# Optimization experiments

Measured on AMD Instinct MI355X. Metric: run time of the kernel, lower is better.

Reference implementation:

```python
import jax, jax.numpy as jnp
import numpy as np

B, S, D = 1, 1024, 1024
NH, DH, DR = 8, 128, 64
DCQ, DC = 768, 256
INTER, E, TOPK = 512, 8, 2

def rmsnorm(x, w, eps=1e-6):
    return x * jax.lax.rsqrt(jnp.mean(x * x, -1, keepdims=True) + eps) * w

def lin(x, w, b):
    return x @ w.T + b

def apply_rope(x, cos, sin):
    # x: [b, s, h, d]; cos/sin: [S, d//2]; complex rotate pairs (even, odd)
    b, s, h, d = x.shape
    xr = x.reshape(b, s, h, d // 2, 2)
    x0, x1 = xr[..., 0], xr[..., 1]
    c = cos[None, :s, None, :]
    sn = sin[None, :s, None, :]
    return jnp.stack([x0 * c - x1 * sn, x0 * sn + x1 * c], -1).reshape(b, s, h, d)

def setup_inputs():
    keys = iter(jax.random.split(jax.random.key(0), 64))
    def nrm(*shape):
        return jax.random.normal(next(keys), shape, jnp.float32) * 0.02
    theta = 1.0 / (10000.0 ** (jnp.arange(0, DR, 2, dtype=jnp.float32) / DR))
    ang = jnp.arange(S, dtype=jnp.float32)[:, None] * theta[None, :]
    return dict(
        h=jax.random.normal(next(keys), (B, S, D), jnp.float32),
        freqs_cos=jnp.cos(ang), freqs_sin=jnp.sin(ang),
        mask=jnp.triu(jnp.ones((S, S), bool), 1),
        attn_norm_w=jnp.ones(D), ffn_norm_w=jnp.ones(D),
        wq_down=nrm(DCQ, D), bq_down=jnp.zeros(DCQ), q_norm_w=jnp.ones(DCQ),
        wqc=nrm(NH * DH, DCQ), bqc=jnp.zeros(NH * DH),
        wqr=nrm(NH * DR, DCQ), bqr=jnp.zeros(NH * DR),
        wkr=nrm(DR, D), bkr=jnp.zeros(DR), kr_norm_w=jnp.ones(DR),
        wkv_down=nrm(DC, D), bkv_down=jnp.zeros(DC), kv_norm_w=jnp.ones(DC),
        wkc=nrm(NH * DH, DC), bkc=jnp.zeros(NH * DH),
        wvc=nrm(NH * DH, DC), bvc=jnp.zeros(NH * DH),
        wo=nrm(D, NH * DH), bo=jnp.zeros(D),
        sw1=nrm(INTER, D), sb1=jnp.zeros(INTER), sw2=nrm(D, INTER), sb2=jnp.zeros(D),
        sw3=nrm(INTER, D), sb3=jnp.zeros(INTER),
        ew1=nrm(E, INTER, D), eb1=jnp.zeros((E, INTER)), ew2=nrm(E, D, INTER), eb2=jnp.zeros((E, D)),
        ew3=nrm(E, INTER, D), eb3=jnp.zeros((E, INTER)),
        centroids=jax.random.normal(next(keys), (E, D), jnp.float32), biases=jnp.zeros(E),
    )

def _forward(h, freqs_cos, freqs_sin, mask, attn_norm_w, ffn_norm_w, wq_down, bq_down, q_norm_w, wqc, bqc, wqr, bqr, wkr, bkr, kr_norm_w, wkv_down, bkv_down, kv_norm_w, wkc, bkc, wvc, bvc, wo, bo, sw1, sb1, sw2, sb2, sw3, sb3, ew1, eb1, ew2, eb2, ew3, eb3, centroids, biases):
    b, s, _ = h.shape
    # --- pre-norm MLA attention ---
    x = rmsnorm(h, attn_norm_w)
    cQ = rmsnorm(lin(x, wq_down, bq_down), q_norm_w)
    qR = apply_rope(lin(cQ, wqr, bqr).reshape(b, s, NH, DR), freqs_cos, freqs_sin)
    qC = lin(cQ, wqc, bqc).reshape(b, s, NH, DH)
    q = jnp.concatenate([qC, qR], -1)                      # [b,s,NH,DH+DR]
    kR = apply_rope(rmsnorm(lin(x, wkr, bkr), kr_norm_w).reshape(b, s, 1, DR), freqs_cos, freqs_sin)
    cKV = rmsnorm(lin(x, wkv_down, bkv_down), kv_norm_w)
    kC = lin(cKV, wkc, bkc).reshape(b, s, NH, DH)
    vC = lin(cKV, wvc, bvc).reshape(b, s, NH, DH)
    k = jnp.concatenate([jnp.broadcast_to(kR, (b, s, NH, DR)), kC], -1)  # source order: [kR, kC]
    scores = jnp.einsum('bqhd,bkhd->bhqk', q, k) / jnp.sqrt(jnp.float32(DH + DR))
    scores = jnp.where(mask[None, None], jnp.finfo(scores.dtype).min, scores)
    attw = jax.nn.softmax(scores, -1)                      # dropout in eval mode = identity
    attn = jnp.einsum('bhqk,bkhd->bqhd', attw, vC).reshape(b, s, NH * DH)
    x1 = h + lin(attn, wo, bo)
    # --- pre-norm MoE FFN ---
    y = rmsnorm(x1, ffn_norm_w)
    shared = lin(jax.nn.silu(lin(y, sw1, sb1)) * lin(y, sw3, sb3), sw2, sb2)  # mean over 1 shared expert
    affinity = jax.nn.sigmoid(y @ centroids.T)             # [b,s,E]
    _, topi = jax.lax.top_k(affinity + biases, TOPK)
    gates = jax.nn.softmax(jnp.take_along_axis(affinity, topi, -1), -1)      # [b,s,TOPK]
    combine = (jax.nn.one_hot(topi, E, dtype=y.dtype) * gates[..., None]).sum(-2)  # [b,s,E]
    h1 = jax.nn.silu(jnp.einsum('bsd,eid->bsei', y, ew1) + eb1) * (jnp.einsum('bsd,eid->bsei', y, ew3) + eb3)
    out_e = jnp.einsum('bsei,edi->bsed', h1, ew2) + eb2
    routed = (out_e * combine[..., None]).sum(2)
    return x1 + shared + routed

def reference(h, freqs_cos, freqs_sin, mask, attn_norm_w, ffn_norm_w, wq_down, bq_down, q_norm_w, wqc, bqc, wqr, bqr, wkr, bkr, kr_norm_w, wkv_down, bkv_down, kv_norm_w, wkc, bkc, wvc, bvc, wo, bo, sw1, sb1, sw2, sb2, sw3, sb3, ew1, eb1, ew2, eb2, ew3, eb3, centroids, biases):
    return _forward(h, freqs_cos, freqs_sin, mask, attn_norm_w, ffn_norm_w, wq_down, bq_down, q_norm_w, wqc, bqc, wqr, bqr, wkr, bkr, kr_norm_w, wkv_down, bkv_down, kv_norm_w, wkc, bkc, wvc, bvc, wo, bo, sw1, sb1, sw2, sb2, sw3, sb3, ew1, eb1, ew2, eb2, ew3, eb3, centroids, biases)
```

## Files before the change

### kernel.cpp

```cpp
#include <hip/hip_runtime.h>

typedef unsigned short u16;
typedef __attribute__((ext_vector_type(8))) short short8;
typedef __attribute__((ext_vector_type(4))) float f32x4;

__device__ __forceinline__ float b2f(u16 u) { return __uint_as_float(((unsigned)u) << 16); }
__device__ __forceinline__ u16 f2b(float f) {
    unsigned x = __float_as_uint(f);
    return (u16)((x + 0x7fffu + ((x >> 16) & 1u)) >> 16);
}

#define GLDS16(gp, lp) __builtin_amdgcn_global_load_lds( \
    (const __attribute__((address_space(1))) void*)(gp), \
    (__attribute__((address_space(3))) void*)(lp), 16, 0, 0)

#define WAITV(N) do { \
    asm volatile("s_waitcnt vmcnt(" #N ")" ::: "memory"); \
    __builtin_amdgcn_sched_barrier(0); \
} while (0)

#define KC8_SWZ(lane) ((((lane) & 3) ^ (((lane) >> 3) & 3)) << 3)
#define RD_SWZ(fm, fq) (((fq) ^ (((fm) >> 1) & 3)) << 3)

__device__ __forceinline__ void xcd_swz(int& bx, int& by) {
    if ((gridDim.x & 7) == 0 && gridDim.y == 16) {
        int lid = bx + by * gridDim.x;
        int q = lid >> 3, r = lid & 7;
        by = q & 15;
        bx = r + ((q >> 4) << 3);
    }
}

struct Seg { const u16* W; const float* bias; void* C; int ldc; int epi; int bx0; int aidx; };
struct GArgs {
    const u16* A[2]; int lda[2]; int K[2];
    Seg seg[4]; int nseg;
    const float* res;
    float* dst2;
};

__launch_bounds__(256)
__global__ void mgemm4(GArgs ga)
{
    __shared__ u16 As[6 * 2048];
    __shared__ u16 Bs[6 * 2048];
    int bx = blockIdx.x, by = blockIdx.y;
    xcd_swz(bx, by);
    int si = 0;
#pragma unroll
    for (int i = 1; i < 4; i++)
        if (i < ga.nseg && bx >= ga.seg[i].bx0) si = i;
    const u16* Wp = ga.seg[si].W;
    const float* bp = ga.seg[si].bias;
    void* Cp = ga.seg[si].C;
    const int ldco = ga.seg[si].ldc;
    const int epi = ga.seg[si].epi;
    const int ai = ga.seg[si].aidx;
    const u16* Ap = ga.A[ai];
    const int lda = ga.lda[ai], K = ga.K[ai];
    const int col0 = (bx - ga.seg[si].bx0) * 64;
    const int row0 = by * 64;

    int tid = threadIdx.x;
    int lane = tid & 63, w = tid >> 6;
    int r0 = (w << 4) + (lane >> 2), kc8 = KC8_SWZ(lane);
    const u16* gA = Ap + (size_t)(row0 + r0) * lda + kc8;
    const u16* gB = Wp + (size_t)(col0 + r0) * lda + kc8;

    int fm = lane & 15, fq = lane >> 4;
    const int so = RD_SWZ(fm, fq);
    f32x4 acc[4] = {};

#define MG_STAGE(BS, KO) do { \
    GLDS16(gA + (KO), As + (BS) * 2048 + (w << 9)); \
    GLDS16(gB + (KO), Bs + (BS) * 2048 + (w << 9)); \
} while (0)

    const int nst = K >> 5;
    MG_STAGE(0, 0); MG_STAGE(1, 32); MG_STAGE(2, 64); MG_STAGE(3, 96);
    int bcur = 0;
    for (int t = 0; t < nst; t += 2) {
        if (t < nst - 2) { WAITV(4); } else { WAITV(0); }
        __builtin_amdgcn_s_barrier();
        int w4 = bcur + 4; if (w4 >= 6) w4 -= 6;
        int w5 = w4 + 1;   if (w5 >= 6) w5 -= 6;
        if (t + 4 < nst) MG_STAGE(w4, (t + 4) << 5);
        if (t + 5 < nst) MG_STAGE(w5, (t + 5) << 5);
#pragma unroll
        for (int sub = 0; sub < 2; sub++) {
            int bc = bcur + sub; if (bc >= 6) bc -= 6;
            short8 af = *(const short8*)(As + bc * 2048 + (w << 9) + fm * 32 + so);
            short8 bf[4];
#pragma unroll
            for (int nt = 0; nt < 4; nt++)
                bf[nt] = *(const short8*)(Bs + bc * 2048 + ((nt << 4) + fm) * 32 + so);
#pragma unroll
            for (int nt = 0; nt < 4; nt++)
                acc[nt] = __builtin_amdgcn_mfma_f32_16x16x32_bf16(af, bf[nt], acc[nt], 0, 0, 0);
        }
        bcur += 2; if (bcur >= 6) bcur -= 6;
    }
#undef MG_STAGE

    int rbase = row0 + (w << 4) + (fq << 2);
#pragma unroll
    for (int nt = 0; nt < 4; nt++) {
        int c = col0 + (nt << 4) + fm;
        float bcol = bp[c];
#pragma unroll
        for (int reg = 0; reg < 4; reg++) {
            int r = rbase + reg;
            float v = acc[nt][reg] + bcol;
            if (epi == 3)
                ((u16*)Cp)[(size_t)r * ldco + c] = f2b(v);
            else if (epi == 1) {
                float o = v + ga.res[(size_t)r * ldco + c];
                ((float*)Cp)[(size_t)r * ldco + c] = o;
                if (ga.dst2) ga.dst2[(size_t)r * ldco + c] = o;
            } else
                ((float*)Cp)[(size_t)r * ldco + c] = v;
        }
    }
}

__launch_bounds__(256)
__global__ void mega_glu(const u16* __restrict__ Y16,
                         const u16* __restrict__ sw1, const float* __restrict__ sb1,
                         const u16* __restrict__ sw3, const float* __restrict__ sb3,
                         const u16* __restrict__ ew1, const float* __restrict__ eb1,
                         const u16* __restrict__ ew3, const float* __restrict__ eb3,
                         u16* __restrict__ Gb,
                         const int* __restrict__ lists, const int* __restrict__ counts)
{
    __shared__ u16 As[6 * 2048];
    __shared__ u16 B1s[6 * 2048];
    __shared__ u16 B3s[6 * 2048];
    int bx = blockIdx.x, by = blockIdx.y, z = blockIdx.z;
    xcd_swz(bx, by);
    int col0 = bx * 64;
    int cnt = 1024; const int* list = nullptr;
    const u16 *W1p, *W3p; const float *b1p, *b3p;
    if (z == 0) {
        W1p = sw1; b1p = sb1; W3p = sw3; b3p = sb3;
    } else {
        int e = z - 1; cnt = counts[e]; list = lists + (e << 10);
        W1p = ew1 + (size_t)e * 512 * 1024; b1p = eb1 + e * 512;
        W3p = ew3 + (size_t)e * 512 * 1024; b3p = eb3 + e * 512;
    }
    int row0 = by * 64;
    if (row0 >= cnt) return;
    u16* Cp = Gb + (size_t)z * 524288;

    int tid = threadIdx.x, lane = tid & 63, w = tid >> 6;
    int r0 = (w << 4) + (lane >> 2), kc8 = KC8_SWZ(lane);
    int ar = row0 + r0;
    if (z > 0) ar = list[ar < cnt ? ar : cnt - 1];
    const u16* gA = Y16 + (size_t)ar * 1024 + kc8;
    const u16* gB1 = W1p + (size_t)(col0 + r0) * 1024 + kc8;
    const u16* gB3 = W3p + (size_t)(col0 + r0) * 1024 + kc8;

    int fm = lane & 15, fq = lane >> 4;
    const int so = RD_SWZ(fm, fq);
    f32x4 accU[4] = {}, accV[4] = {};

#define GL_STAGE(BS, KO) do { \
    GLDS16(gA + (KO),  As  + (BS) * 2048 + (w << 9)); \
    GLDS16(gB1 + (KO), B1s + (BS) * 2048 + (w << 9)); \
    GLDS16(gB3 + (KO), B3s + (BS) * 2048 + (w << 9)); \
} while (0)

    GL_STAGE(0, 0); GL_STAGE(1, 32); GL_STAGE(2, 64); GL_STAGE(3, 96);
    int bcur = 0;
    for (int t = 0; t < 32; t += 2) {
        if (t < 30) { WAITV(6); } else { WAITV(0); }
        __builtin_amdgcn_s_barrier();
        int w4 = bcur + 4; if (w4 >= 6) w4 -= 6;
        int w5 = w4 + 1;   if (w5 >= 6) w5 -= 6;
        if (t + 4 < 32) GL_STAGE(w4, (t + 4) << 5);
        if (t + 5 < 32) GL_STAGE(w5, (t + 5) << 5);
#pragma unroll
        for (int sub = 0; sub < 2; sub++) {
            int bc = bcur + sub; if (bc >= 6) bc -= 6;
            short8 af = *(const short8*)(As + bc * 2048 + (w << 9) + fm * 32 + so);
#pragma unroll
            for (int nt = 0; nt < 4; nt++) {
                short8 b1 = *(const short8*)(B1s + bc * 2048 + ((nt << 4) + fm) * 32 + so);
                accU[nt] = __builtin_amdgcn_mfma_f32_16x16x32_bf16(af, b1, accU[nt], 0, 0, 0);
            }
#pragma unroll
            for (int nt = 0; nt < 4; nt++) {
                short8 b3 = *(const short8*)(B3s + bc * 2048 + ((nt << 4) + fm) * 32 + so);
                accV[nt] = __builtin_amdgcn_mfma_f32_16x16x32_bf16(af, b3, accV[nt], 0, 0, 0);
            }
        }
        bcur += 2; if (bcur >= 6) bcur -= 6;
    }
#undef GL_STAGE

    int rbase = row0 + (w << 4) + (fq << 2);
#pragma unroll
    for (int nt = 0; nt < 4; nt++) {
        int c = col0 + (nt << 4) + fm;
        float b1c = b1p[c], b3c = b3p[c];
#pragma unroll
        for (int reg = 0; reg < 4; reg++) {
            int r = rbase + reg;
            if (r >= cnt) continue;
            float u = b2f(f2b(accU[nt][reg] + b1c));
            float v = b2f(f2b(accV[nt][reg] + b3c));
            Cp[(size_t)r * 512 + c] = f2b(u / (1.f + __expf(-u)) * v);
        }
    }
}

__launch_bounds__(256)
__global__ void mega_down(const u16* __restrict__ Gb,
                          const u16* __restrict__ sw2, const float* __restrict__ sb2,
                          const u16* __restrict__ ew2, const float* __restrict__ eb2,
                          float* __restrict__ Dscr,
                          const int* __restrict__ counts)
{
    __shared__ u16 Gs[6 * 2048];
    __shared__ u16 Ws[6 * 2048];
    int bx = blockIdx.x, by = blockIdx.y, z = blockIdx.z;
    xcd_swz(bx, by);
    int cnt = 1024;
    const u16* Wp; const float* bp;
    if (z == 0) { Wp = sw2; bp = sb2; }
    else {
        int e = z - 1;
        cnt = counts[e];
        Wp = ew2 + (size_t)e * 1024 * 512; bp = eb2 + e * 1024;
    }
    int row0 = by * 64;
    if (row0 >= cnt) return;
    const u16* Ap = Gb + (size_t)z * 524288;
    int col0 = bx * 64;
    float* Dp = Dscr + (size_t)z * 1048576;

    int tid = threadIdx.x, lane = tid & 63, w = tid >> 6;
    int r0 = (w << 4) + (lane >> 2), kc8 = KC8_SWZ(lane);
    const u16* gG = Ap + (size_t)(row0 + r0) * 512 + kc8;
    const u16* gW = Wp + (size_t)(col0 + r0) * 512 + kc8;

    int fm = lane & 15, fq = lane >> 4;
    const int so = RD_SWZ(fm, fq);
    f32x4 acc[4] = {};

#define MD_STAGE(BS, KO) do { \
    GLDS16(gG + (KO), Gs + (BS) * 2048 + (w << 9)); \
    GLDS16(gW + (KO), Ws + (BS) * 2048 + (w << 9)); \
} while (0)

    MD_STAGE(0, 0); MD_STAGE(1, 32); MD_STAGE(2, 64); MD_STAGE(3, 96);
    int bcur = 0;
    for (int t = 0; t < 16; t += 2) {
        if (t < 14) { WAITV(4); } else { WAITV(0); }
        __builtin_amdgcn_s_barrier();
        int w4 = bcur + 4; if (w4 >= 6) w4 -= 6;
        int w5 = w4 + 1;   if (w5 >= 6) w5 -= 6;
        if (t + 4 < 16) MD_STAGE(w4, (t + 4) << 5);
        if (t + 5 < 16) MD_STAGE(w5, (t + 5) << 5);
#pragma unroll
        for (int sub = 0; sub < 2; sub++) {
            int bc = bcur + sub; if (bc >= 6) bc -= 6;
            short8 af = *(const short8*)(Gs + bc * 2048 + (w << 9) + fm * 32 + so);
            short8 bf[4];
#pragma unroll
            for (int nt = 0; nt < 4; nt++)
                bf[nt] = *(const short8*)(Ws + bc * 2048 + ((nt << 4) + fm) * 32 + so);
#pragma unroll
            for (int nt = 0; nt < 4; nt++)
                acc[nt] = __builtin_amdgcn_mfma_f32_16x16x32_bf16(af, bf[nt], acc[nt], 0, 0, 0);
        }
        bcur += 2; if (bcur >= 6) bcur -= 6;
    }
#undef MD_STAGE

    int rbase = row0 + (w << 4) + (fq << 2);
#pragma unroll
    for (int nt = 0; nt < 4; nt++) {
        int c = col0 + (nt << 4) + fm;
        float bcol = bp[c];
#pragma unroll
        for (int reg = 0; reg < 4; reg++) {
            int r = rbase + reg;
            Dp[(size_t)r * 1024 + c] = acc[nt][reg] + bcol;
        }
    }
}

__launch_bounds__(256)
__global__ void ffn_combine(const float* __restrict__ Dscr,
                            const int* __restrict__ sE, const int* __restrict__ sP,
                            const float* __restrict__ sG,
                            float* __restrict__ out)
{
    int t = blockIdx.x, tid = threadIdx.x;
    int e0 = sE[t * 2], e1 = sE[t * 2 + 1];
    int p0 = sP[t * 2], p1 = sP[t * 2 + 1];
    float g0 = sG[t * 2], g1 = sG[t * 2 + 1];
    const float4* Ds = (const float4*)(Dscr + (size_t)t * 1024);
    const float4* D0 = (const float4*)(Dscr + (size_t)(e0 + 1) * 1048576 + (size_t)p0 * 1024);
    const float4* D1 = (const float4*)(Dscr + (size_t)(e1 + 1) * 1048576 + (size_t)p1 * 1024);
    float4* o = (float4*)(out + (size_t)t * 1024);
    float4 a = o[tid], s = Ds[tid], x0 = D0[tid], x1 = D1[tid];
    a.x += s.x + g0 * x0.x + g1 * x1.x;
    a.y += s.y + g0 * x0.y + g1 * x1.y;
    a.z += s.z + g0 * x0.z + g1 * x1.z;
    a.w += s.w + g0 * x0.w + g1 * x1.w;
    o[tid] = a;
}

__launch_bounds__(256)
__global__ void attn_mfma(const u16* __restrict__ Qp, const u16* __restrict__ Kp,
                          const u16* __restrict__ VT,
                          float* __restrict__ Opart, float* __restrict__ MLp)
{
    const int qt = blockIdx.x, h = blockIdx.y, z = blockIdx.z;
    const int q0 = qt * 64;
    const int tid = threadIdx.x;
    const int lane = tid & 63, w = tid >> 6;
    const int fm = lane & 15, fq = lane >> 4;

    __shared__ u16 Ks[12288];
    __shared__ u16 Vs[8192];
    __shared__ u16 Ps[4096];

    const u16* qrow = Qp + ((size_t)h * 1024 + q0 + w * 16 + fm) * 192;
    short8 qf[6];
#pragma unroll
    for (int c = 0; c < 6; c++)
        qf[c] = *(const short8*)(qrow + c * 32 + fq * 8);

    const u16* Kb = Kp + (size_t)h * 1024 * 192;
    const u16* Vb = VT + (size_t)h * 128 * 1024;

    float m_i[4], l_i[4];
#pragma unroll
    for (int r = 0; r < 4; r++) { m_i[r] = -1e30f; l_i[r] = 0.f; }
    f32x4 accO[8] = {};
    const float scale = 0.07216878364870323f;
    const int nt64 = qt + 1;
    const int ktlo = (z * nt64) >> 2;
    const int kthi = ((z + 1) * nt64) >> 2;
    const int rbase = w * 16 + fq * 4;

    for (int kt = ktlo; kt < kthi; ++kt) {
        const int o = kt * 64;
#pragma unroll
        for (int i = 0; i < 6; i++) {
            int idx = w + 4 * i;
            int c = idx >> 2, k4 = idx & 3;
            const u16* g = Kb + (size_t)(o + k4 * 16 + (lane >> 2)) * 192 + c * 32 + (lane & 3) * 8;
            GLDS16(g, Ks + c * 2048 + k4 * 512 + lane * 8);
        }
#pragma unroll
        for (int i = 0; i < 4; i++) {
            int idx = w + 4 * i;
            int kc = idx >> 3, k8 = idx & 7;
            const u16* g = Vb + (size_t)(k8 * 16 + (lane >> 2)) * 1024 + o + kc * 32 + (lane & 3) * 8;
            GLDS16(g, Vs + kc * 4096 + k8 * 512 + lane * 8);
        }
        __syncthreads();
        f32x4 sacc[4];
        __builtin_amdgcn_s_setprio(1);
#pragma unroll
        for (int nt = 0; nt < 4; nt++) {
            sacc[nt] = (f32x4){0.f, 0.f, 0.f, 0.f};
#pragma unroll
            for (int c = 0; c < 6; c++) {
                short8 kf = *(const short8*)(Ks + c * 2048 + (nt * 16 + fm) * 32 + fq * 8);
                sacc[nt] = __builtin_amdgcn_mfma_f32_16x16x32_bf16(qf[c], kf, sacc[nt], 0, 0, 0);
            }
        }
        __builtin_amdgcn_s_setprio(0);
        float pv[4][4], rmax[4];
#pragma unroll
        for (int reg = 0; reg < 4; reg++) {
            int q = q0 + rbase + reg;
            float mx = -1e30f;
#pragma unroll
            for (int nt = 0; nt < 4; nt++) {
                int gk = o + nt * 16 + fm;
                float s = sacc[nt][reg] * scale;
                if (gk > q) s = -1e30f;
                pv[nt][reg] = s;
                mx = fmaxf(mx, s);
            }
            rmax[reg] = mx;
        }
#pragma unroll
        for (int m = 1; m < 16; m <<= 1)
#pragma unroll
            for (int reg = 0; reg < 4; reg++)
                rmax[reg] = fmaxf(rmax[reg], __shfl_xor(rmax[reg], m));
        float alpha[4], rsum[4];
#pragma unroll
        for (int reg = 0; reg < 4; reg++) {
            float mn = fmaxf(m_i[reg], rmax[reg]);
            alpha[reg] = __expf(m_i[reg] - mn);
            m_i[reg] = mn;
// ... 149 lines not shown
            if (tid == 0) aff[e] = 1.f / (1.f + expf(-red[0] * scale));
            __syncthreads();
        }
        if (tid == 0) {
            float sb[8];
#pragma unroll
            for (int e = 0; e < 8; e++) sb[e] = aff[e] + biases[e];
            int i0 = 0;
            for (int e = 1; e < 8; e++) if (sb[e] > sb[i0]) i0 = e;
            int i1 = -1;
            for (int e = 0; e < 8; e++) { if (e == i0) continue; if (i1 < 0 || sb[e] > sb[i1]) i1 = e; }
            float a0 = aff[i0], a1 = aff[i1];
            float mx = fmaxf(a0, a1);
            float e0 = expf(a0 - mx), e1 = expf(a1 - mx);
            float inv = 1.f / (e0 + e1);
            int p0 = atomicAdd(&counts[i0], 1);
            lists[i0 * 1024 + p0] = t;
            int p1 = atomicAdd(&counts[i1], 1);
            lists[i1 * 1024 + p1] = t;
            sE[t * 2] = i0; sP[t * 2] = p0; sG[t * 2] = e0 * inv;
            sE[t * 2 + 1] = i1; sP[t * 2 + 1] = p1; sG[t * 2 + 1] = e1 * inv;
        }
    }
}

__launch_bounds__(256)
__global__ void pack_all(const float* __restrict__ QC, const float* __restrict__ QRr,
                         const float* __restrict__ KRraw, const float* __restrict__ krw,
                         const float* __restrict__ KC,
                         const u16* __restrict__ VCb,
                         const float* __restrict__ fcos, const float* __restrict__ fsin,
                         u16* __restrict__ Qp, u16* __restrict__ Kp, u16* __restrict__ VT)
{
    __shared__ u16 Ts[64][68];
    __shared__ float kshared[64];
    int b = blockIdx.x, tid = threadIdx.x;
    if (b < 1024) {
        int s = b;
        if (tid < 64) {
            float v = KRraw[(size_t)s * 64 + tid];
            float ss = v * v;
#pragma unroll
            for (int m = 1; m < 64; m <<= 1) ss += __shfl_xor(ss, m);
            float scale = rsqrtf(ss / 64.f + 1e-6f);
            int j = tid >> 1;
            float c = fcos[s * 32 + j], sn = fsin[s * 32 + j];
            float x0 = KRraw[(size_t)s * 64 + (tid & ~1)] * scale * krw[tid & ~1];
            float x1 = KRraw[(size_t)s * 64 + (tid | 1)]  * scale * krw[tid | 1];
            kshared[tid] = (tid & 1) ? (x0 * sn + x1 * c) : (x0 * c - x1 * sn);
        }
        __syncthreads();
        for (int e = tid; e < 1536; e += 256) {
            int h = e / 192, d = e % 192;
            float q;
            if (d < 128) {
                q = QC[(size_t)s * 1024 + h * 128 + d];
            } else {
                int dd = d - 128, j = dd >> 1;
                float c = fcos[s * 32 + j], sn = fsin[s * 32 + j];
                float x0 = QRr[(size_t)s * 512 + h * 64 + (dd & ~1)];
                float x1 = QRr[(size_t)s * 512 + h * 64 + (dd | 1)];
                q = (dd & 1) ? (x0 * sn + x1 * c) : (x0 * c - x1 * sn);
            }
            Qp[((size_t)h * 1024 + s) * 192 + d] = f2b(q);
            float k = (d < 64) ? kshared[d]
                               : KC[(size_t)s * 1024 + h * 128 + d - 64];
            Kp[((size_t)h * 1024 + s) * 192 + d] = f2b(k);
        }
    } else {
        int idx = b - 1024;
        int s0 = (idx & 15) * 64, d0 = (idx >> 4) * 64;
        for (int k = 0; k < 16; k++) {
            int e = tid + k * 256, r = e >> 6, c = e & 63;
            Ts[r][c] = VCb[(size_t)(s0 + r) * 1024 + d0 + c];
        }
        __syncthreads();
        for (int k = 0; k < 16; k++) {
            int e = tid + k * 256, d = e >> 6, s = e & 63;
            VT[(size_t)(d0 + d) * 1024 + s0 + s] = Ts[s][d];
        }
    }
}

#define NCAST 4096
__launch_bounds__(256)
__global__ void fused_cast(const float* p0, const float* p1, const float* p2,
                           const float* p3, const float* p4, const float* p5,
                           const float* p6, const float* p7, const float* p8,
                           const float* p9, const float* p10, const float* p11,
                           const float* p12, const float* pkr,
                           u16* __restrict__ dst,
                           const float* __restrict__ hX, const float* __restrict__ attnw,
                           u16* __restrict__ X16, int* __restrict__ zc)
{
    __shared__ float red[256];
    int b = blockIdx.x, tid = threadIdx.x;
    if (b < NCAST) {
        const int NQ = 18022400 / 4;
        for (int i = b * 256 + tid; i < NQ; i += NCAST * 256) {
            int e = i * 4;
            const float* s; int base;
            if      (e <   786432) { s = p0;  base = 0; }
            else if (e <  1048576) { s = p1;  base =   786432; }
            else if (e <  1835008) { s = p2;  base =  1048576; }
            else if (e <  2228224) { s = p3;  base =  1835008; }
            else if (e <  2490368) { s = p4;  base =  2228224; }
            else if (e <  2752512) { s = p5;  base =  2490368; }
            else if (e <  3801088) { s = p6;  base =  2752512; }
            else if (e <  4325376) { s = p7;  base =  3801088; }
            else if (e <  4849664) { s = p8;  base =  4325376; }
            else if (e <  5373952) { s = p9;  base =  4849664; }
            else if (e <  9568256) { s = p10; base =  5373952; }
            else if (e < 13762560) { s = p11; base =  9568256; }
            else if (e < 17956864) { s = p12; base = 13762560; }
            else                   { s = pkr; base = 17956864; }
            float4 v = *(const float4*)(s + (e - base));
            ushort4 o;
            o.x = f2b(v.x); o.y = f2b(v.y); o.z = f2b(v.z); o.w = f2b(v.w);
            *(ushort4*)(dst + e) = o;
        }
    } else {
        int r = b - NCAST;
        if (r == 0 && tid < 8) zc[tid] = 0;
        const float* xr = hX + (size_t)r * 1024;
        float ss = 0.f;
        for (int j = tid; j < 1024; j += 256) { float v = xr[j]; ss += v * v; }
        red[tid] = ss; __syncthreads();
        for (int st = 128; st > 0; st >>= 1) { if (tid < st) red[tid] += red[tid + st]; __syncthreads(); }
        float scale = rsqrtf(red[0] / 1024.f + 1e-6f);
        for (int j = tid; j < 1024; j += 256)
            X16[(size_t)r * 1024 + j] = f2b(xr[j] * scale * attnw[j]);
    }
}

extern "C" void kernel_launch(void* const* d_in, const int* in_sizes, int n_in,
                              void* d_out, int out_size, void* d_ws, size_t ws_size,
                              hipStream_t stream)
{
    (void)in_sizes; (void)n_in; (void)ws_size; (void)out_size;
    const float* h       = (const float*)d_in[0];
    const float* fcos    = (const float*)d_in[1];
    const float* fsin    = (const float*)d_in[2];
    const float* attn_w  = (const float*)d_in[4];
    const float* ffn_w   = (const float*)d_in[5];
    const float* wq_down = (const float*)d_in[6];
    const float* bq_down = (const float*)d_in[7];
    const float* q_norm  = (const float*)d_in[8];
    const float* wqc     = (const float*)d_in[9];
    const float* bqc     = (const float*)d_in[10];
    const float* wqr     = (const float*)d_in[11];
    const float* bqr     = (const float*)d_in[12];
    const float* wkr     = (const float*)d_in[13];
    const float* bkr     = (const float*)d_in[14];
    const float* kr_norm = (const float*)d_in[15];
    const float* wkv     = (const float*)d_in[16];
    const float* bkv     = (const float*)d_in[17];
    const float* kv_norm = (const float*)d_in[18];
    const float* wkc     = (const float*)d_in[19];
    const float* bkc     = (const float*)d_in[20];
    const float* wvc     = (const float*)d_in[21];
    const float* bvc     = (const float*)d_in[22];
    const float* wo      = (const float*)d_in[23];
    const float* bo      = (const float*)d_in[24];
    const float* sw1     = (const float*)d_in[25];
    const float* sb1     = (const float*)d_in[26];
    const float* sw2     = (const float*)d_in[27];
    const float* sb2     = (const float*)d_in[28];
    const float* sw3     = (const float*)d_in[29];
    const float* sb3     = (const float*)d_in[30];
    const float* ew1     = (const float*)d_in[31];
    const float* eb1     = (const float*)d_in[32];
    const float* ew2     = (const float*)d_in[33];
    const float* eb2     = (const float*)d_in[34];
    const float* ew3     = (const float*)d_in[35];
    const float* eb3     = (const float*)d_in[36];
    const float* cent    = (const float*)d_in[37];
    const float* biases  = (const float*)d_in[38];

    char* wsb = (char*)d_ws;
    const size_t U5 = 512 * 1024;
    u16*   X16   = (u16*)(wsb + 8 * U5);
    float* QRr   = (float*)(wsb + 12 * U5);
    float* CQraw = (float*)(wsb + 16 * U5);
    u16*   ATT16 = (u16*)(wsb + 16 * U5);
    u16*   CQ16  = (u16*)(wsb + 22 * U5);
    float* CKVraw= (float*)(wsb + 25 * U5);
    u16*   CKV16 = (u16*)(wsb + 27 * U5);
    float* KRraw = (float*)(wsb + 28 * U5);
    float* QC    = (float*)(wsb + 29 * U5);
    float* KC    = (float*)(wsb + 37 * U5);
    float* X1    = (float*)(wsb + 53 * U5);
    int*   counts= (int*)(wsb + 61 * U5 + 64 * 1024);
    int*   lists = (int*)(wsb + 61 * U5 + 32 * 1024);
    int*   sE    = (int*)(wsb + 61 * U5 + 72 * 1024);
    int*   sP    = (int*)(wsb + 61 * U5 + 80 * 1024);
    float* sG    = (float*)(wsb + 61 * U5 + 88 * 1024);
    u16*   Y16   = (u16*)(wsb + 69 * U5);
    u16*   Gb    = (u16*)(wsb + 73 * U5);

    u16* wb = (u16*)(wsb + 92 * U5);
    u16 *c_wq  = wb;
    u16 *c_wkv = c_wq  + 786432;
    u16 *c_wqc = c_wkv + 262144;
    u16 *c_wqr = c_wqc + 786432;
    u16 *c_wkc = c_wqr + 393216;
    u16 *c_wvc = c_wkc + 262144;
    u16 *c_wo  = c_wvc + 262144;
    u16 *c_sw1 = c_wo  + 1048576;
    u16 *c_sw3 = c_sw1 + 524288;
    u16 *c_sw2 = c_sw3 + 524288;
    u16 *c_ew1 = c_sw2 + 524288;
    u16 *c_ew3 = c_ew1 + 4194304;
    u16 *c_ew2 = c_ew3 + 4194304;
    u16 *c_wkr = c_ew2 + 4194304;
    u16* VCb = (u16*)(wsb + 92 * U5 + 36175872);
    u16* VTp = VCb + 1048576;
    u16* Qpk = VTp + 1048576;
    u16* Kpk = Qpk + 1572864;
    float* Opart = (float*)(wsb + 192 * U5);
    float* Dscr  = (float*)(wsb + 224 * U5);
    float* MLp   = (float*)(wsb + 296 * U5);

    fused_cast<<<NCAST + 1024, 256, 0, stream>>>(wq_down, wkv, wqc, wqr, wkc, wvc, wo,
                                                 sw1, sw3, sw2, ew1, ew3, ew2, wkr, wb,
                                                 h, attn_w, X16, counts);

    {
        GArgs g = {};
        g.A[0] = X16; g.lda[0] = 1024; g.K[0] = 1024;
        g.seg[0] = { c_wq,  bq_down, CQraw,  768, 0, 0,  0 };
        g.seg[1] = { c_wkv, bkv,     CKVraw, 256, 0, 12, 0 };
        g.seg[2] = { c_wkr, bkr,     KRraw,  64,  0, 16, 0 };
        g.nseg = 3;
        mgemm4<<<dim3(17, 16), 256, 0, stream>>>(g);
    }
    rmsnorm2x<<<2048, 256, 0, stream>>>(CQraw, q_norm, CQ16, 768,
                                        CKVraw, kv_norm, CKV16, 256);
    {
        GArgs g = {};
        g.A[0] = CQ16;  g.lda[0] = 768; g.K[0] = 768;
        g.A[1] = CKV16; g.lda[1] = 256; g.K[1] = 256;
        g.seg[0] = { c_wqc, bqc, QC,   1024, 0, 0,  0 };
        g.seg[1] = { c_wqr, bqr, QRr,  512,  0, 16, 0 };
        g.seg[2] = { c_wkc, bkc, KC,   1024, 0, 24, 1 };
        g.seg[3] = { c_wvc, bvc, VCb,  1024, 3, 40, 1 };
        g.nseg = 4;
        mgemm4<<<dim3(56, 16), 256, 0, stream>>>(g);
    }
    pack_all<<<1280, 256, 0, stream>>>(QC, QRr, KRraw, kr_norm, KC, VCb, fcos, fsin,
                                       Qpk, Kpk, VTp);
    attn_mfma<<<dim3(16, 8, 4), 256, 0, stream>>>(Qpk, Kpk, VTp, Opart, MLp);
    attn_combine4<<<512, 256, 0, stream>>>(Opart, MLp, ATT16);
    {
        GArgs g = {};
        g.A[0] = ATT16; g.lda[0] = 1024; g.K[0] = 1024;
        g.seg[0] = { c_wo, bo, X1, 1024, 1, 0, 0 };
        g.nseg = 1; g.res = h; g.dst2 = (float*)d_out;
        mgemm4<<<dim3(16, 16), 256, 0, stream>>>(g);
    }

    rmsnorm_route<<<2048, 256, 0, stream>>>(X1, ffn_w, Y16, cent, biases,
                                            counts, lists, sE, sP, sG);
    mega_glu<<<dim3(8, 16, 9), 256, 0, stream>>>(Y16, c_sw1, sb1, c_sw3, sb3,
                                                 c_ew1, eb1, c_ew3, eb3,
                                                 Gb, lists, counts);
    mega_down<<<dim3(16, 16, 9), 256, 0, stream>>>(Gb, c_sw2, sb2, c_ew2, eb2,
                                                   Dscr, counts);
    ffn_combine<<<1024, 256, 0, stream>>>(Dscr, sE, sP, sG, (float*)d_out);
}
```

Measured before the change: 341.8 us.

## Enlarge GEMM tiles to 128 rows and switch to 4-stage single-step pipeline

```diff
diff --git a/kernel.cpp b/kernel.cpp
--- a/kernel.cpp
+++ b/kernel.cpp
@@ -23,11 +23,11 @@
 #define RD_SWZ(fm, fq) (((fq) ^ (((fm) >> 1) & 3)) << 3)
 
 __device__ __forceinline__ void xcd_swz(int& bx, int& by) {
-    if ((gridDim.x & 7) == 0 && gridDim.y == 16) {
+    if ((gridDim.x & 7) == 0 && gridDim.y == 8) {
         int lid = bx + by * gridDim.x;
         int q = lid >> 3, r = lid & 7;
-        by = q & 15;
-        bx = r + ((q >> 4) << 3);
+        by = q & 7;
+        bx = r + ((q >> 3) << 3);
     }
 }
 
@@ -42,8 +42,8 @@
 __launch_bounds__(256)
 __global__ void mgemm4(GArgs ga)
 {
-    __shared__ u16 As[6 * 2048];
-    __shared__ u16 Bs[6 * 2048];
+    __shared__ u16 As[4 * 4096];
+    __shared__ u16 Bs[4 * 2048];
     int bx = blockIdx.x, by = blockIdx.y;
     xcd_swz(bx, by);
     int si = 0;
@@ -59,66 +59,73 @@
     const u16* Ap = ga.A[ai];
     const int lda = ga.lda[ai], K = ga.K[ai];
     const int col0 = (bx - ga.seg[si].bx0) * 64;
-    const int row0 = by * 64;
+    const int row0 = by * 128;
 
     int tid = threadIdx.x;
     int lane = tid & 63, w = tid >> 6;
-    int r0 = (w << 4) + (lane >> 2), kc8 = KC8_SWZ(lane);
-    const u16* gA = Ap + (size_t)(row0 + r0) * lda + kc8;
-    const u16* gB = Wp + (size_t)(col0 + r0) * lda + kc8;
+    int rr = lane >> 2, kc8 = KC8_SWZ(lane);
+    const u16* gA0 = Ap + (size_t)(row0 + (w << 4) + rr) * lda + kc8;
+    const u16* gA1 = gA0 + (size_t)64 * lda;
+    const u16* gB  = Wp + (size_t)(col0 + (w << 4) + rr) * lda + kc8;
 
     int fm = lane & 15, fq = lane >> 4;
     const int so = RD_SWZ(fm, fq);
-    f32x4 acc[4] = {};
+    f32x4 acc[2][4] = {};
 
 #define MG_STAGE(BS, KO) do { \
-    GLDS16(gA + (KO), As + (BS) * 2048 + (w << 9)); \
-    GLDS16(gB + (KO), Bs + (BS) * 2048 + (w << 9)); \
+    GLDS16(gA0 + (KO), As + (BS) * 4096 + (w << 9)); \
+    GLDS16(gA1 + (KO), As + (BS) * 4096 + 2048 + (w << 9)); \
+    GLDS16(gB  + (KO), Bs + (BS) * 2048 + (w << 9)); \
 } while (0)
 
     const int nst = K >> 5;
-    MG_STAGE(0, 0); MG_STAGE(1, 32); MG_STAGE(2, 64); MG_STAGE(3, 96);
-    int bcur = 0;
-    for (int t = 0; t < nst; t += 2) {
-        if (t < nst - 2) { WAITV(4); } else { WAITV(0); }
+    MG_STAGE(0, 0); MG_STAGE(1, 32); MG_STAGE(2, 64);
+    int bc = 0;
+    for (int t = 0; t < nst; t++) {
+        if (t < nst - 2) { WAITV(6); }
+        else if (t == nst - 2) { WAITV(3); }
+        else { WAITV(0); }
         __builtin_amdgcn_s_barrier();
-        int w4 = bcur + 4; if (w4 >= 6) w4 -= 6;
-        int w5 = w4 + 1;   if (w5 >= 6) w5 -= 6;
-        if (t + 4 < nst) MG_STAGE(w4, (t + 4) << 5);
-        if (t + 5 < nst) MG_STAGE(w5, (t + 5) << 5);
-#pragma unroll
-        for (int sub = 0; sub < 2; sub++) {
-            int bc = bcur + sub; if (bc >= 6) bc -= 6;
-            short8 af = *(const short8*)(As + bc * 2048 + (w << 9) + fm * 32 + so);
-            short8 bf[4];
+        if (t + 3 < nst) {
+            int bs = bc + 3; if (bs >= 4) bs -= 4;
+            MG_STAGE(bs, (t + 3) << 5);
+        }
+        short8 af[2], bf[4];
+#pragma unroll
+        for (int mt = 0; mt < 2; mt++)
+            af[mt] = *(const short8*)(As + bc * 4096 + ((w << 5) + (mt << 4) + fm) * 32 + so);
+#pragma unroll
+        for (int nt = 0; nt < 4; nt++)
+            bf[nt] = *(const short8*)(Bs + bc * 2048 + ((nt << 4) + fm) * 32 + so);
+#pragma unroll
+        for (int mt = 0; mt < 2; mt++)
 #pragma unroll
             for (int nt = 0; nt < 4; nt++)
-                bf[nt] = *(const short8*)(Bs + bc * 2048 + ((nt << 4) + fm) * 32 + so);
-#pragma unroll
-            for (int nt = 0; nt < 4; nt++)
-                acc[nt] = __builtin_amdgcn_mfma_f32_16x16x32_bf16(af, bf[nt], acc[nt], 0, 0, 0);
-        }
-        bcur += 2; if (bcur >= 6) bcur -= 6;
+                acc[mt][nt] = __builtin_amdgcn_mfma_f32_16x16x32_bf16(af[mt], bf[nt], acc[mt][nt], 0, 0, 0);
+        bc = (bc + 1) & 3;
     }
 #undef MG_STAGE
 
-    int rbase = row0 + (w << 4) + (fq << 2);
-#pragma unroll
-    for (int nt = 0; nt < 4; nt++) {
-        int c = col0 + (nt << 4) + fm;
-        float bcol = bp[c];
-#pragma unroll
-        for (int reg = 0; reg < 4; reg++) {
-            int r = rbase + reg;
-            float v = acc[nt][reg] + bcol;
-            if (epi == 3)
-                ((u16*)Cp)[(size_t)r * ldco + c] = f2b(v);
-            else if (epi == 1) {
-                float o = v + ga.res[(size_t)r * ldco + c];
-                ((float*)Cp)[(size_t)r * ldco + c] = o;
-                if (ga.dst2) ga.dst2[(size_t)r * ldco + c] = o;
-            } else
-                ((float*)Cp)[(size_t)r * ldco + c] = v;
+#pragma unroll
+    for (int mt = 0; mt < 2; mt++) {
+        int rbase = row0 + (w << 5) + (mt << 4) + (fq << 2);
+#pragma unroll
+        for (int nt = 0; nt < 4; nt++) {
+            int c = col0 + (nt << 4) + fm;
+            float bcol = bp[c];
+#pragma unroll
+            for (int reg = 0; reg < 4; reg++) {
+                int r = rbase + reg;
+                float v = acc[mt][nt][reg] + bcol;
+                if (epi == 3)
+                    ((u16*)Cp)[(size_t)r * ldco + c] = f2b(v);
+                else if (epi == 1) {
+                    float o = v + ga.res[(size_t)r * ldco + c];
+                    ((float*)Cp)[(size_t)r * ldco + c] = o;
+                    if (ga.dst2) ga.dst2[(size_t)r * ldco + c] = o;
+                } else
+                    ((float*)Cp)[(size_t)r * ldco + c] = v;
+            }
         }
     }
 }
@@ -132,9 +139,9 @@
                          u16* __restrict__ Gb,
                          const int* __restrict__ lists, const int* __restrict__ counts)
 {
-    __shared__ u16 As[6 * 2048];
-    __shared__ u16 B1s[6 * 2048];
-    __shared__ u16 B3s[6 * 2048];
+    __shared__ u16 As[4 * 4096];
+    __shared__ u16 B1s[4 * 2048];
+    __shared__ u16 B3s[4 * 2048];
     int bx = blockIdx.x, by = blockIdx.y, z = blockIdx.z;
     xcd_swz(bx, by);
     int col0 = bx * 64;
@@ -147,68 +154,80 @@
         W1p = ew1 + (size_t)e * 512 * 1024; b1p = eb1 + e * 512;
         W3p = ew3 + (size_t)e * 512 * 1024; b3p = eb3 + e * 512;
     }
-    int row0 = by * 64;
+    int row0 = by * 128;
     if (row0 >= cnt) return;
     u16* Cp = Gb + (size_t)z * 524288;
 
     int tid = threadIdx.x, lane = tid & 63, w = tid >> 6;
-    int r0 = (w << 4) + (lane >> 2), kc8 = KC8_SWZ(lane);
-    int ar = row0 + r0;
-    if (z > 0) ar = list[ar < cnt ? ar : cnt - 1];
-    const u16* gA = Y16 + (size_t)ar * 1024 + kc8;
-    const u16* gB1 = W1p + (size_t)(col0 + r0) * 1024 + kc8;
-    const u16* gB3 = W3p + (size_t)(col0 + r0) * 1024 + kc8;
+    int rr = lane >> 2, kc8 = KC8_SWZ(lane);
+    int ar0 = row0 + (w << 4) + rr;
+    int ar1 = ar0 + 64;
+    if (z > 0) {
+        ar0 = list[ar0 < cnt ? ar0 : cnt - 1];
+        ar1 = list[ar1 < cnt ? ar1 : cnt - 1];
+    }
+    const u16* gA0 = Y16 + (size_t)ar0 * 1024 + kc8;
+    const u16* gA1 = Y16 + (size_t)ar1 * 1024 + kc8;
+    const u16* gB1 = W1p + (size_t)(col0 + (w << 4) + rr) * 1024 + kc8;
+    const u16* gB3 = W3p + (size_t)(col0 + (w << 4) + rr) * 1024 + kc8;
 
     int fm = lane & 15, fq = lane >> 4;
     const int so = RD_SWZ(fm, fq);
-    f32x4 accU[4] = {}, accV[4] = {};
+    f32x4 accU[2][4] = {}, accV[2][4] = {};
 
 #define GL_STAGE(BS, KO) do { \
-    GLDS16(gA + (KO),  As  + (BS) * 2048 + (w << 9)); \
+    GLDS16(gA0 + (KO), As + (BS) * 4096 + (w << 9)); \
+    GLDS16(gA1 + (KO), As + (BS) * 4096 + 2048 + (w << 9)); \
     GLDS16(gB1 + (KO), B1s + (BS) * 2048 + (w << 9)); \
     GLDS16(gB3 + (KO), B3s + (BS) * 2048 + (w << 9)); \
 } while (0)
 
-    GL_STAGE(0, 0); GL_STAGE(1, 32); GL_STAGE(2, 64); GL_STAGE(3, 96);
-    int bcur = 0;
-    for (int t = 0; t < 32; t += 2) {
-        if (t < 30) { WAITV(6); } else { WAITV(0); }
+    GL_STAGE(0, 0); GL_STAGE(1, 32); GL_STAGE(2, 64);
+    int bc = 0;
+    for (int t = 0; t < 32; t++) {
+        if (t < 30) { WAITV(8); }
+        else if (t == 30) { WAITV(4); }
+        else { WAITV(0); }
         __builtin_amdgcn_s_barrier();
-        int w4 = bcur + 4; if (w4 >= 6) w4 -= 6;
-        int w5 = w4 + 1;   if (w5 >= 6) w5 -= 6;
-        if (t + 4 < 32) GL_STAGE(w4, (t + 4) << 5);
-        if (t + 5 < 32) GL_STAGE(w5, (t + 5) << 5);
-#pragma unroll
-        for (int sub = 0; sub < 2; sub++) {
-            int bc = bcur + sub; if (bc >= 6) bc -= 6;
-            short8 af = *(const short8*)(As + bc * 2048 + (w << 9) + fm * 32 + so);
-#pragma unroll
-            for (int nt = 0; nt < 4; nt++) {
-                short8 b1 = *(const short8*)(B1s + bc * 2048 + ((nt << 4) + fm) * 32 + so);
-                accU[nt] = __builtin_amdgcn_mfma_f32_16x16x32_bf16(af, b1, accU[nt], 0, 0, 0);
+        if (t + 3 < 32) {
+            int bs = bc + 3; if (bs >= 4) bs -= 4;
+            GL_STAGE(bs, (t + 3) << 5);
+        }
+        short8 af[2];
+#pragma unroll
+        for (int mt = 0; mt < 2; mt++)
+            af[mt] = *(const short8*)(As + bc * 4096 + ((w << 5) + (mt << 4) + fm) * 32 + so);
+#pragma unroll
+        for (int nt = 0; nt < 4; nt++) {
+            short8 b1 = *(const short8*)(B1s + bc * 2048 + ((nt << 4) + fm) * 32 + so);
+            accU[0][nt] = __builtin_amdgcn_mfma_f32_16x16x32_bf16(af[0], b1, accU[0][nt], 0, 0, 0);
+            accU[1][nt] = __builtin_amdgcn_mfma_f32_16x16x32_bf16(af[1], b1, accU[1][nt], 0, 0, 0);
+        }
+#pragma unroll
+        for (int nt = 0; nt < 4; nt++) {
+            short8 b3 = *(const short8*)(B3s + bc * 2048 + ((nt << 4) + fm) * 32 + so);
+            accV[0][nt] = __builtin_amdgcn_mfma_f32_16x16x32_bf16(af[0], b3, accV[0][nt], 0, 0, 0);
+            accV[1][nt] = __builtin_amdgcn_mfma_f32_16x16x32_bf16(af[1], b3, accV[1][nt], 0, 0, 0);
+        }
+        bc = (bc + 1) & 3;
+    }
+#undef GL_STAGE
+
+#pragma unroll
+    for (int mt = 0; mt < 2; mt++) {
+        int rbase = row0 + (w << 5) + (mt << 4) + (fq << 2);
+#pragma unroll
+        for (int nt = 0; nt < 4; nt++) {
+            int c = col0 + (nt << 4) + fm;
+            float b1c = b1p[c], b3c = b3p[c];
+#pragma unroll
+            for (int reg = 0; reg < 4; reg++) {
+                int r = rbase + reg;
+                if (r >= cnt) continue;
+                float u = b2f(f2b(accU[mt][nt][reg] + b1c));
+                float v = b2f(f2b(accV[mt][nt][reg] + b3c));
+                Cp[(size_t)r * 512 + c] = f2b(u / (1.f + __expf(-u)) * v);
             }
-#pragma unroll
-            for (int nt = 0; nt < 4; nt++) {
-                short8 b3 = *(const short8*)(B3s + bc * 2048 + ((nt << 4) + fm) * 32 + so);
-                accV[nt] = __builtin_amdgcn_mfma_f32_16x16x32_bf16(af, b3, accV[nt], 0, 0, 0);
-            }
-        }
-        bcur += 2; if (bcur >= 6) bcur -= 6;
-    }
-#undef GL_STAGE
-
-    int rbase = row0 + (w << 4) + (fq << 2);
-#pragma unroll
-    for (int nt = 0; nt < 4; nt++) {
-        int c = col0 + (nt << 4) + fm;
-        float b1c = b1p[c], b3c = b3p[c];
-#pragma unroll
-        for (int reg = 0; reg < 4; reg++) {
-            int r = rbase + reg;
-            if (r >= cnt) continue;
-            float u = b2f(f2b(accU[nt][reg] + b1c));
-            float v = b2f(f2b(accV[nt][reg] + b3c));
-            Cp[(size_t)r * 512 + c] = f2b(u / (1.f + __expf(-u)) * v);
         }
     }
 }
@@ -220,8 +239,8 @@
                           float* __restrict__ Dscr,
                           const int* __restrict__ counts)
 {
-    __shared__ u16 Gs[6 * 2048];
-    __shared__ u16 Ws[6 * 2048];
+    __shared__ u16 Gs[4 * 4096];
+    __shared__ u16 Ws[4 * 2048];
     int bx = blockIdx.x, by = blockIdx.y, z = blockIdx.z;
     xcd_swz(bx, by);
     int cnt = 1024;
@@ -232,60 +251,67 @@
         cnt = counts[e];
         Wp = ew2 + (size_t)e * 1024 * 512; bp = eb2 + e * 1024;
     }
-    int row0 = by * 64;
+    int row0 = by * 128;
     if (row0 >= cnt) return;
     const u16* Ap = Gb + (size_t)z * 524288;
     int col0 = bx * 64;
     float* Dp = Dscr + (size_t)z * 1048576;
 
     int tid = threadIdx.x, lane = tid & 63, w = tid >> 6;
-    int r0 = (w << 4) + (lane >> 2), kc8 = KC8_SWZ(lane);
-    const u16* gG = Ap + (size_t)(row0 + r0) * 512 + kc8;
-    const u16* gW = Wp + (size_t)(col0 + r0) * 512 + kc8;
+    int rr = lane >> 2, kc8 = KC8_SWZ(lane);
+    const u16* gG0 = Ap + (size_t)(row0 + (w << 4) + rr) * 512 + kc8;
+    const u16* gG1 = gG0 + (size_t)64 * 512;
+    const u16* gW  = Wp + (size_t)(col0 + (w << 4) + rr) * 512 + kc8;
 
     int fm = lane & 15, fq = lane >> 4;
     const int so = RD_SWZ(fm, fq);
-    f32x4 acc[4] = {};
+    f32x4 acc[2][4] = {};
 
 #define MD_STAGE(BS, KO) do { \
-    GLDS16(gG + (KO), Gs + (BS) * 2048 + (w << 9)); \
-    GLDS16(gW + (KO), Ws + (BS) * 2048 + (w << 9)); \
+    GLDS16(gG0 + (KO), Gs + (BS) * 4096 + (w << 9)); \
+    GLDS16(gG1 + (KO), Gs + (BS) * 4096 + 2048 + (w << 9)); \
+    GLDS16(gW  + (KO), Ws + (BS) * 2048 + (w << 9)); \
 } while (0)
 
-    MD_STAGE(0, 0); MD_STAGE(1, 32); MD_STAGE(2, 64); MD_STAGE(3, 96);
-    int bcur = 0;
-    for (int t = 0; t < 16; t += 2) {
-        if (t < 14) { WAITV(4); } else { WAITV(0); }
+    MD_STAGE(0, 0); MD_STAGE(1, 32); MD_STAGE(2, 64);
+    int bc = 0;
+    for (int t = 0; t < 16; t++) {
+        if (t < 14) { WAITV(6); }
+        else if (t == 14) { WAITV(3); }
+        else { WAITV(0); }
         __builtin_amdgcn_s_barrier();
-        int w4 = bcur + 4; if (w4 >= 6) w4 -= 6;
-        int w5 = w4 + 1;   if (w5 >= 6) w5 -= 6;
-        if (t + 4 < 16) MD_STAGE(w4, (t + 4) << 5);
-        if (t + 5 < 16) MD_STAGE(w5, (t + 5) << 5);
-#pragma unroll
-        for (int sub = 0; sub < 2; sub++) {
-            int bc = bcur + sub; if (bc >= 6) bc -= 6;
-            short8 af = *(const short8*)(Gs + bc * 2048 + (w << 9) + fm * 32 + so);
-            short8 bf[4];
+        if (t + 3 < 16) {
+            int bs = bc + 3; if (bs >= 4) bs -= 4;
+            MD_STAGE(bs, (t + 3) << 5);
+        }
+        short8 af[2], bf[4];
+#pragma unroll
+        for (int mt = 0; mt < 2; mt++)
+            af[mt] = *(const short8*)(Gs + bc * 4096 + ((w << 5) + (mt << 4) + fm) * 32 + so);
+#pragma unroll
+        for (int nt = 0; nt < 4; nt++)
+            bf[nt] = *(const short8*)(Ws + bc * 2048 + ((nt << 4) + fm) * 32 + so);
+#pragma unroll
+        for (int mt = 0; mt < 2; mt++)
 #pragma unroll
             for (int nt = 0; nt < 4; nt++)
-                bf[nt] = *(const short8*)(Ws + bc * 2048 + ((nt << 4) + fm) * 32 + so);
-#pragma unroll
-            for (int nt = 0; nt < 4; nt++)
-                acc[nt] = __builtin_amdgcn_mfma_f32_16x16x32_bf16(af, bf[nt], acc[nt], 0, 0, 0);
-        }
-        bcur += 2; if (bcur >= 6) bcur -= 6;
+                acc[mt][nt] = __builtin_amdgcn_mfma_f32_16x16x32_bf16(af[mt], bf[nt], acc[mt][nt], 0, 0, 0);
+        bc = (bc + 1) & 3;
     }
 #undef MD_STAGE
 
-    int rbase = row0 + (w << 4) + (fq << 2);
-#pragma unroll
-    for (int nt = 0; nt < 4; nt++) {
-        int c = col0 + (nt << 4) + fm;
-        float bcol = bp[c];
-#pragma unroll
-        for (int reg = 0; reg < 4; reg++) {
-            int r = rbase + reg;
-            Dp[(size_t)r * 1024 + c] = acc[nt][reg] + bcol;
+#pragma unroll
+    for (int mt = 0; mt < 2; mt++) {
+        int rbase = row0 + (w << 5) + (mt << 4) + (fq << 2);
+#pragma unroll
+        for (int nt = 0; nt < 4; nt++) {
+            int c = col0 + (nt << 4) + fm;
+            float bcol = bp[c];
+#pragma unroll
+            for (int reg = 0; reg < 4; reg++) {
+                int r = rbase + reg;
+                Dp[(size_t)r * 1024 + c] = acc[mt][nt][reg] + bcol;
+            }
         }
     }
 }
@@ -783,7 +809,7 @@
         g.seg[1] = { c_wkv, bkv,     CKVraw, 256, 0, 12, 0 };
         g.seg[2] = { c_wkr, bkr,     KRraw,  64,  0, 16, 0 };
         g.nseg = 3;
-        mgemm4<<<dim3(17, 16), 256, 0, stream>>>(g);
+        mgemm4<<<dim3(17, 8), 256, 0, stream>>>(g);
     }
     rmsnorm2x<<<2048, 256, 0, stream>>>(CQraw, q_norm, CQ16, 768,
                                         CKVraw, kv_norm, CKV16, 256);
@@ -796,7 +822,7 @@
         g.seg[2] = { c_wkc, bkc, KC,   1024, 0, 24, 1 };
         g.seg[3] = { c_wvc, bvc, VCb,  1024, 3, 40, 1 };
         g.nseg = 4;
-        mgemm4<<<dim3(56, 16), 256, 0, stream>>>(g);
+        mgemm4<<<dim3(56, 8), 256, 0, stream>>>(g);
     }
     pack_all<<<1280, 256, 0, stream>>>(QC, QRr, KRraw, kr_norm, KC, VCb, fcos, fsin,
                                        Qpk, Kpk, VTp);
@@ -807,15 +833,15 @@
         g.A[0] = ATT16; g.lda[0] = 1024; g.K[0] = 1024;
         g.seg[0] = { c_wo, bo, X1, 1024, 1, 0, 0 };
         g.nseg = 1; g.res = h; g.dst2 = (float*)d_out;
-        mgemm4<<<dim3(16, 16), 256, 0, stream>>>(g);
+        mgemm4<<<dim3(16, 8), 256, 0, stream>>>(g);
     }
 
     rmsnorm_route<<<2048, 256, 0, stream>>>(X1, ffn_w, Y16, cent, biases,
                                             counts, lists, sE, sP, sG);
-    mega_glu<<<dim3(8, 16, 9), 256, 0, stream>>>(Y16, c_sw1, sb1, c_sw3, sb3,
-                                                 c_ew1, eb1, c_ew3, eb3,
-                                                 Gb, lists, counts);
-    mega_down<<<dim3(16, 16, 9), 256, 0, stream>>>(Gb, c_sw2, sb2, c_ew2, eb2,
-                                                   Dscr, counts);
+    mega_glu<<<dim3(8, 8, 9), 256, 0, stream>>>(Y16, c_sw1, sb1, c_sw3, sb3,
+                                                c_ew1, eb1, c_ew3, eb3,
+                                                Gb, lists, counts);
+    mega_down<<<dim3(16, 8, 9), 256, 0, stream>>>(Gb, c_sw2, sb2, c_ew2, eb2,
+                                                  Dscr, counts);
     ffn_combine<<<1024, 256, 0, stream>>>(Dscr, sE, sP, sG, (float*)d_out);
 }
```

Measured after the change: 364.0 us. 6.5% more time.

## Overlap FFN weight bf16 casting with attention kernel via extra blocks

Applied to the files above, without the earlier changes.

```diff
diff --git a/kernel.cpp b/kernel.cpp
--- a/kernel.cpp
+++ b/kernel.cpp
@@ -315,9 +315,32 @@
 __launch_bounds__(256)
 __global__ void attn_mfma(const u16* __restrict__ Qp, const u16* __restrict__ Kp,
                           const u16* __restrict__ VT,
-                          float* __restrict__ Opart, float* __restrict__ MLp)
+                          float* __restrict__ Opart, float* __restrict__ MLp,
+                          const float* __restrict__ fsw1, const float* __restrict__ fsw3,
+                          const float* __restrict__ fsw2, const float* __restrict__ few1,
+                          const float* __restrict__ few3, const float* __restrict__ few2,
+                          u16* __restrict__ warena)
 {
     const int qt = blockIdx.x, h = blockIdx.y, z = blockIdx.z;
+    if (z >= 4) {
+        int cb = (z - 4) * 128 + h * 16 + qt;
+        const int NQ4 = (17956864 - 3801088) / 4;
+        for (int i = cb * 256 + threadIdx.x; i < NQ4; i += 1024 * 256) {
+            int e = 3801088 + i * 4;
+            const float* s; int base;
+            if      (e <  4325376) { s = fsw1; base =  3801088; }
+            else if (e <  4849664) { s = fsw3; base =  4325376; }
+            else if (e <  5373952) { s = fsw2; base =  4849664; }
+            else if (e <  9568256) { s = few1; base =  5373952; }
+            else if (e < 13762560) { s = few3; base =  9568256; }
+            else                   { s = few2; base = 13762560; }
+            float4 v = *(const float4*)(s + (e - base));
+            ushort4 o;
+            o.x = f2b(v.x); o.y = f2b(v.y); o.z = f2b(v.z); o.w = f2b(v.w);
+            *(ushort4*)(warena + e) = o;
+        }
+        return;
+    }
     const int q0 = qt * 64;
     const int tid = threadIdx.x;
     const int lane = tid & 63, w = tid >> 6;
@@ -633,13 +656,11 @@
     }
 }
 
-#define NCAST 4096
+#define NCAST 1024
 __launch_bounds__(256)
 __global__ void fused_cast(const float* p0, const float* p1, const float* p2,
                            const float* p3, const float* p4, const float* p5,
-                           const float* p6, const float* p7, const float* p8,
-                           const float* p9, const float* p10, const float* p11,
-                           const float* p12, const float* pkr,
+                           const float* p6, const float* pkr,
                            u16* __restrict__ dst,
                            const float* __restrict__ hX, const float* __restrict__ attnw,
                            u16* __restrict__ X16, int* __restrict__ zc)
@@ -647,28 +668,22 @@
     __shared__ float red[256];
     int b = blockIdx.x, tid = threadIdx.x;
     if (b < NCAST) {
-        const int NQ = 18022400 / 4;
+        const int NQ = 3866624 / 4;
         for (int i = b * 256 + tid; i < NQ; i += NCAST * 256) {
             int e = i * 4;
-            const float* s; int base;
-            if      (e <   786432) { s = p0;  base = 0; }
-            else if (e <  1048576) { s = p1;  base =   786432; }
-            else if (e <  1835008) { s = p2;  base =  1048576; }
-            else if (e <  2228224) { s = p3;  base =  1835008; }
-            else if (e <  2490368) { s = p4;  base =  2228224; }
-            else if (e <  2752512) { s = p5;  base =  2490368; }
-            else if (e <  3801088) { s = p6;  base =  2752512; }
-            else if (e <  4325376) { s = p7;  base =  3801088; }
-            else if (e <  4849664) { s = p8;  base =  4325376; }
-            else if (e <  5373952) { s = p9;  base =  4849664; }
-            else if (e <  9568256) { s = p10; base =  5373952; }
-            else if (e < 13762560) { s = p11; base =  9568256; }
-            else if (e < 17956864) { s = p12; base = 13762560; }
-            else                   { s = pkr; base = 17956864; }
+            const float* s; int base; int dstoff;
+            if      (e <   786432) { s = p0;  base = 0;       dstoff = e; }
+            else if (e <  1048576) { s = p1;  base =  786432; dstoff = e; }
+            else if (e <  1835008) { s = p2;  base = 1048576; dstoff = e; }
+            else if (e <  2228224) { s = p3;  base = 1835008; dstoff = e; }
+            else if (e <  2490368) { s = p4;  base = 2228224; dstoff = e; }
+            else if (e <  2752512) { s = p5;  base = 2490368; dstoff = e; }
+            else if (e <  3801088) { s = p6;  base = 2752512; dstoff = e; }
+            else { s = pkr; base = 3801088; dstoff = 17956864 + (e - 3801088); }
             float4 v = *(const float4*)(s + (e - base));
             ushort4 o;
             o.x = f2b(v.x); o.y = f2b(v.y); o.z = f2b(v.z); o.w = f2b(v.w);
-            *(ushort4*)(dst + e) = o;
+            *(ushort4*)(dst + dstoff) = o;
         }
     } else {
         int r = b - NCAST;
@@ -773,8 +788,7 @@
     float* MLp   = (float*)(wsb + 296 * U5);
 
     fused_cast<<<NCAST + 1024, 256, 0, stream>>>(wq_down, wkv, wqc, wqr, wkc, wvc, wo,
-                                                 sw1, sw3, sw2, ew1, ew3, ew2, wkr, wb,
-                                                 h, attn_w, X16, counts);
+                                                 wkr, wb, h, attn_w, X16, counts);
 
     {
         GArgs g = {};
@@ -800,7 +814,8 @@
     }
     pack_all<<<1280, 256, 0, stream>>>(QC, QRr, KRraw, kr_norm, KC, VCb, fcos, fsin,
                                        Qpk, Kpk, VTp);
-    attn_mfma<<<dim3(16, 8, 4), 256, 0, stream>>>(Qpk, Kpk, VTp, Opart, MLp);
+    attn_mfma<<<dim3(16, 8, 12), 256, 0, stream>>>(Qpk, Kpk, VTp, Opart, MLp,
+                                                   sw1, sw3, sw2, ew1, ew3, ew2, wb);
     attn_combine4<<<512, 256, 0, stream>>>(Opart, MLp, ATT16);
     {
         GArgs g = {};
```

New measurement: 344.8 us. Within noise of the previous version (+0.9%).
